# Kernel tuning notes

Hardware: AMD Instinct MI355X
Metric: run time of the kernel (lower is better)

## Reference

```python
import jax, jax.numpy as jnp
import numpy as np

DIM = 512
HEADS = 8
HEAD_DIM = DIM // HEADS
SCALE = HEAD_DIM ** -0.5
GROUP1 = np.array([2, 3, 5, 6, 1, 4, 0, 7, 8, 9, 14, 15, 11, 12, 10, 13])
GROUP2 = np.array([0, 1, 2, 3, 5, 6, 4, 7])
EPS = 1e-5


def setup_inputs() -> dict:
    key = jax.random.key(0)
    ks = jax.random.split(key, 6)
    B, N, C = 4096, 16, DIM
    x = jax.random.normal(ks[0], (B, N, C), dtype=jnp.float32)
    w_q = jax.random.normal(ks[1], (C, C), dtype=jnp.float32) * 0.02
    w_kv = jax.random.normal(ks[2], (2 * C, C), dtype=jnp.float32) * 0.02
    w_proj = jax.random.normal(ks[3], (C, C), dtype=jnp.float32) * 0.02
    b_proj = jax.random.normal(ks[4], (C,), dtype=jnp.float32) * 0.02
    gamma = jnp.ones((C,), dtype=jnp.float32)
    beta = jnp.zeros((C,), dtype=jnp.float32)
    return {"x": x, "w_q": w_q, "w_kv": w_kv, "w_proj": w_proj,
            "b_proj": b_proj, "gamma": gamma, "beta": beta}


def _layernorm(x, gamma, beta):
    mu = jnp.mean(x, axis=-1, keepdims=True)
    var = jnp.mean(jnp.square(x - mu), axis=-1, keepdims=True)
    return (x - mu) * jax.lax.rsqrt(var + EPS) * gamma + beta


def _avg_pool_pairs(x):
    # x: (B, L, C) -> (B, L//2, C), AvgPool1d(kernel=2, stride=2) over L
    return 0.5 * (x[:, 0::2] + x[:, 1::2])


def reference(x, w_q, w_kv, w_proj, b_proj, gamma, beta):
    B, N, C = x.shape
    q = (x @ w_q.T).reshape(B, N, HEADS, HEAD_DIM).transpose(0, 2, 1, 3)  # (B,H,N,d)
    # gather + avgpool preprocessing
    p1 = _avg_pool_pairs(x[:, GROUP1])  # (B, 8, C)
    p2 = _avg_pool_pairs(x[:, GROUP2])  # (B, 4, C)
    pools = jnp.concatenate([x, p1, p2], axis=1)  # (B, N+12, C)
    pools = _layernorm(pools, gamma, beta)
    M = pools.shape[1]
    kv = (pools @ w_kv.T).reshape(B, M, 2, HEADS, HEAD_DIM).transpose(2, 0, 3, 1, 4)
    k, v = kv[0], kv[1]  # (B,H,M,d)
    attn = jax.nn.softmax(jnp.einsum('bhnd,bhmd->bhnm', q, k) * SCALE, axis=-1)
    out = jnp.einsum('bhnm,bhmd->bhnd', attn, v)  # (B,H,N,d)
    out = out.transpose(0, 2, 1, 3).reshape(B, N, C)
    return out @ w_proj.T + b_proj
```

## Files before the change

kernel.cpp:

```cpp
#include <hip/hip_runtime.h>
#include <hip/hip_bf16.h>
#include <cstdint>
#include <cstddef>


using bf16 = __hip_bfloat16;

#define B_SZ   4096
#define NTOK   16
#define CDIM   512
#define MPOOL  28
#define NHEAD  8
#define HDIM   64
#define LN_EPS 1e-5f
#define ATT_SCALE 0.125f

typedef short bf16x8 __attribute__((ext_vector_type(8)));
typedef float f32x4  __attribute__((ext_vector_type(4)));

__constant__ int c_g1[16] = {2,3,5,6,1,4,0,7,8,9,14,15,11,12,10,13};
__constant__ int c_g2[8]  = {0,1,2,3,5,6,4,7};

__device__ __forceinline__ unsigned short f2b(float f) {
    unsigned u = __float_as_uint(f);
    return (unsigned short)((u + 0x7FFFu + ((u >> 16) & 1u)) >> 16);
}

__device__ __forceinline__ void lds_cp16(const void* g, void* l) {
    __builtin_amdgcn_global_load_lds(
        (const __attribute__((address_space(1))) void*)g,
        (__attribute__((address_space(3))) void*)l, 16, 0, 0);
}

__global__ __launch_bounds__(256) void f32_to_bf16_kernel(
    const float* __restrict__ src, bf16* __restrict__ dst, int n8)
{
    const int i = blockIdx.x * 256 + threadIdx.x;
    if (i >= n8) return;
    const float4* p = (const float4*)(src + (size_t)i * 8);
    float4 a = p[0], b = p[1];
    uint4 pk;
    pk.x = (unsigned)f2b(a.x) | ((unsigned)f2b(a.y) << 16);
    pk.y = (unsigned)f2b(a.z) | ((unsigned)f2b(a.w) << 16);
    pk.z = (unsigned)f2b(b.x) | ((unsigned)f2b(b.y) << 16);
    pk.w = (unsigned)f2b(b.z) | ((unsigned)f2b(b.w) << 16);
    *(uint4*)(dst + (size_t)i * 8) = pk;
}

__global__ __launch_bounds__(256) void pools_ln_kernel(
    const float* __restrict__ x, const float* __restrict__ gamma,
    const float* __restrict__ beta, bf16* __restrict__ pools,
    bf16* __restrict__ xb)
{
    const int wave = threadIdx.x >> 6;
    const int lane = threadIdx.x & 63;
    const int row  = blockIdx.x * 4 + wave;
    const int b = row / MPOOL;
    const int m = row % MPOOL;
    const float* xb_src = x + (size_t)b * NTOK * CDIM;
    const int c0 = lane * 8;

    float v[8];
    if (m < 16) {
        const float4* p = (const float4*)(xb_src + m * CDIM + c0);
        float4 a = p[0], c = p[1];
        v[0]=a.x; v[1]=a.y; v[2]=a.z; v[3]=a.w;
        v[4]=c.x; v[5]=c.y; v[6]=c.z; v[7]=c.w;
        uint4 pk;
        pk.x = (unsigned)f2b(v[0]) | ((unsigned)f2b(v[1]) << 16);
        pk.y = (unsigned)f2b(v[2]) | ((unsigned)f2b(v[3]) << 16);
        pk.z = (unsigned)f2b(v[4]) | ((unsigned)f2b(v[5]) << 16);
        pk.w = (unsigned)f2b(v[6]) | ((unsigned)f2b(v[7]) << 16);
        *(uint4*)(xb + (size_t)b * NTOK * CDIM + (size_t)m * CDIM + c0) = pk;
    } else {
        int r0, r1;
        if (m < 24) { int j = m - 16; r0 = c_g1[2*j]; r1 = c_g1[2*j+1]; }
        else        { int j = m - 24; r0 = c_g2[2*j]; r1 = c_g2[2*j+1]; }
        const float4* p0 = (const float4*)(xb_src + r0 * CDIM + c0);
        const float4* p1 = (const float4*)(xb_src + r1 * CDIM + c0);
        float4 a0 = p0[0], a1 = p0[1];
        float4 b0 = p1[0], b1 = p1[1];
        v[0]=0.5f*(a0.x+b0.x); v[1]=0.5f*(a0.y+b0.y);
        v[2]=0.5f*(a0.z+b0.z); v[3]=0.5f*(a0.w+b0.w);
        v[4]=0.5f*(a1.x+b1.x); v[5]=0.5f*(a1.y+b1.y);
        v[6]=0.5f*(a1.z+b1.z); v[7]=0.5f*(a1.w+b1.w);
    }

    float s = 0.f, sq = 0.f;
#pragma unroll
    for (int j = 0; j < 8; ++j) { s += v[j]; sq += v[j]*v[j]; }
#pragma unroll
    for (int off = 1; off < 64; off <<= 1) {
        s  += __shfl_xor(s,  off, 64);
        sq += __shfl_xor(sq, off, 64);
    }
    const float mu   = s * (1.f / CDIM);
    const float var  = sq * (1.f / CDIM) - mu * mu;
    const float rstd = rsqrtf(var + LN_EPS);

    unsigned short o[8];
#pragma unroll
    for (int j = 0; j < 8; ++j) {
        float g  = gamma[c0 + j];
        float bb = beta[c0 + j];
        o[j] = f2b((v[j] - mu) * rstd * g + bb);
    }
    uint4 pk;
    pk.x = (unsigned)o[0] | ((unsigned)o[1] << 16);
    pk.y = (unsigned)o[2] | ((unsigned)o[3] << 16);
    pk.z = (unsigned)o[4] | ((unsigned)o[5] << 16);
    pk.w = (unsigned)o[6] | ((unsigned)o[7] << 16);
    *(uint4*)(pools + (size_t)row * CDIM + c0) = pk;
}

template<bool OUT_BF16, bool BIAS, int NBLK>
__global__ __launch_bounds__(512, 2) void gemm256_kernel(
    const bf16* __restrict__ A, const bf16* __restrict__ W,
    const float* __restrict__ bias, void* __restrict__ Cptr, int Ncols)
{
    constexpr int K  = 512;
    constexpr int NT = K / 32;
    extern __shared__ __align__(16) char ring[];

    const int tid = threadIdx.x;
    const int wv = tid >> 6, ln = tid & 63;
    const int wr = wv >> 2, wc = wv & 3;
    const int fr = ln & 15, kb = ln >> 4;

    const int p  = blockIdx.x;
    const int o  = p >> 3;
    const int mb = (o / NBLK) * 8 + (p & 7);
    const int nb = o % NBLK;
    const size_t m0 = (size_t)mb * 256;
    const size_t n0 = (size_t)nb * 256;

    const int srow = wv * 16 + (ln >> 2);
    const int scol = (((ln & 3) * 16) ^ (((ln >> 3) & 3) << 4)) >> 1;
    const bf16* Asrc0 = A + (m0 + srow) * K + scol;
    const bf16* Asrc1 = A + (m0 + 128 + srow) * K + scol;
    const bf16* Wsrc0 = W + (n0 + srow) * K + scol;
    const bf16* Wsrc1 = W + (n0 + 128 + srow) * K + scol;
    char* const ringc = ring;

    const int aswz  = ((fr >> 1) & 3) << 4;
    const int a_off = (wr * 128 + fr) * 64 + ((kb * 16) ^ aswz);
    const int b_off = 16384 + (wc * 64 + fr) * 64 + ((kb * 16) ^ aswz);

    f32x4 acc[8][4];
#pragma unroll
    for (int i = 0; i < 8; ++i)
#pragma unroll
    for (int j = 0; j < 4; ++j)
        acc[i][j] = f32x4{0.f, 0.f, 0.f, 0.f};

    auto STAGE = [&](int t) {
        char* base = ringc + (t & 3) * 32768 + wv * 1024;
        const int ko = t * 32;
        lds_cp16(Asrc0 + ko, base);
        lds_cp16(Asrc1 + ko, base + 8192);
        lds_cp16(Wsrc0 + ko, base + 16384);
        lds_cp16(Wsrc1 + ko, base + 16384 + 8192);
    };

    STAGE(0);
    STAGE(1);
    asm volatile("s_waitcnt vmcnt(4)" ::: "memory");
    __builtin_amdgcn_s_barrier();

#pragma unroll 1
    for (int t = 0; t < NT; ++t) {
        if (t + 2 < NT) STAGE(t + 2);
        const char* sa = ringc + (t & 3) * 32768;

        bf16x8 af[8], bfr[4];
#pragma unroll
        for (int mi = 0; mi < 8; ++mi)
            af[mi] = *(const bf16x8*)(sa + a_off + mi * 1024);
#pragma unroll
        for (int nj = 0; nj < 4; ++nj)
            bfr[nj] = *(const bf16x8*)(sa + b_off + nj * 1024);

#pragma unroll
        for (int mi = 0; mi < 8; ++mi)
#pragma unroll
        for (int nj = 0; nj < 4; ++nj)
            acc[mi][nj] = __builtin_amdgcn_mfma_f32_16x16x32_bf16(
                af[mi], bfr[nj], acc[mi][nj], 0, 0, 0);

        if (t + 2 < NT) { asm volatile("s_waitcnt vmcnt(4)" ::: "memory"); }
        else            { asm volatile("s_waitcnt vmcnt(0)" ::: "memory"); }
        __builtin_amdgcn_s_barrier();
    }

    const int orow0 = wr * 128 + kb * 4;
    const int ocol0 = wc * 64 + fr;
    float bv[4];
#pragma unroll
    for (int nj = 0; nj < 4; ++nj)
        bv[nj] = BIAS ? bias[n0 + ocol0 + nj * 16] : 0.f;
#pragma unroll
    for (int mi = 0; mi < 8; ++mi) {
        const size_t rbase = m0 + orow0 + mi * 16;
#pragma unroll
        for (int r = 0; r < 4; ++r) {
            const size_t rowoff = (rbase + r) * (size_t)Ncols + n0 + ocol0;
#pragma unroll
            for (int nj = 0; nj < 4; ++nj) {
                float v = acc[mi][nj][r] + bv[nj];
                if (OUT_BF16)
                    ((unsigned short*)Cptr)[rowoff + nj * 16] = f2b(v);
                else
                    ((float*)Cptr)[rowoff + nj * 16] = v;
            }
        }
    }
}

__global__ __launch_bounds__(256) void attn_kernel(
    const bf16* __restrict__ q, const bf16* __restrict__ kv,
    bf16* __restrict__ att)
{
    __shared__ unsigned short P_t[4][512];

    const int tid = threadIdx.x;
    const int wv = tid >> 6, ln = tid & 63;
    const int fr = ln & 15, kb = ln >> 4;
    const int wg = blockIdx.x * 4 + wv;
    const int b = wg >> 3, h = wg & 7;

    const bf16* qb = q  + (size_t)b * (NTOK * CDIM) + h * HDIM;
    const bf16* kp = kv + (size_t)b * (MPOOL * 2 * CDIM) + h * HDIM;
    const bf16* vp = kp + CDIM;

    bf16x8 aq[2];
#pragma unroll
    for (int ks = 0; ks < 2; ++ks)
        aq[ks] = *(const bf16x8*)(qb + fr * CDIM + ks * 32 + kb * 8);

    bf16x8 bk[2][2];
#pragma unroll
    for (int mt = 0; mt < 2; ++mt)
#pragma unroll
        for (int ks = 0; ks < 2; ++ks)
            bk[mt][ks] = *(const bf16x8*)(kp + (size_t)(mt * 16 + fr) * (2 * CDIM)
                                             + ks * 32 + kb * 8);

    const bf16* vlane = vp + (size_t)kb * 8 * (2 * CDIM) + fr;
    bf16x8 bv[4];
#pragma unroll
    for (int dt = 0; dt < 4; ++dt)
#pragma unroll
        for (int j = 0; j < 8; ++j)
            bv[dt][j] = *(const short*)(vlane + (size_t)j * (2 * CDIM) + dt * 16);

    f32x4 st0 = {0.f, 0.f, 0.f, 0.f}, st1 = {0.f, 0.f, 0.f, 0.f};
    st0 = __builtin_amdgcn_mfma_f32_16x16x32_bf16(aq[0], bk[0][0], st0, 0, 0, 0);
    st0 = __builtin_amdgcn_mfma_f32_16x16x32_bf16(aq[1], bk[0][1], st0, 0, 0, 0);
    st1 = __builtin_amdgcn_mfma_f32_16x16x32_bf16(aq[0], bk[1][0], st1, 0, 0, 0);
    st1 = __builtin_amdgcn_mfma_f32_16x16x32_bf16(aq[1], bk[1][1], st1, 0, 0, 0);

    const bool kmask = (fr >= MPOOL - 16);
#pragma unroll
    for (int r = 0; r < 4; ++r) {
        st0[r] *= ATT_SCALE;
        st1[r] = kmask ? -1e30f : st1[r] * ATT_SCALE;
    }

    float p0[4], p1[4];
#pragma unroll
    for (int r = 0; r < 4; ++r) {
        float mx = fmaxf(st0[r], st1[r]);
        mx = fmaxf(mx, __shfl_xor(mx, 1, 64));
        mx = fmaxf(mx, __shfl_xor(mx, 2, 64));
        mx = fmaxf(mx, __shfl_xor(mx, 4, 64));
        mx = fmaxf(mx, __shfl_xor(mx, 8, 64));
        float e0 = expf(st0[r] - mx);
        float e1 = expf(st1[r] - mx);
        float s = e0 + e1;
        s += __shfl_xor(s, 1, 64);
        s += __shfl_xor(s, 2, 64);
        s += __shfl_xor(s, 4, 64);
        s += __shfl_xor(s, 8, 64);
        const float inv = 1.f / s;
        p0[r] = e0 * inv;
        p1[r] = e1 * inv;
    }

    {
        ushort4 w0, w1;
        w0.x = f2b(p0[0]); w0.y = f2b(p0[1]); w0.z = f2b(p0[2]); w0.w = f2b(p0[3]);
        w1.x = f2b(p1[0]); w1.y = f2b(p1[1]); w1.z = f2b(p1[2]); w1.w = f2b(p1[3]);
        *(ushort4*)&P_t[wv][(fr)      * 16 + kb * 4] = w0;
        *(ushort4*)&P_t[wv][(16 + fr) * 16 + kb * 4] = w1;
    }
    asm volatile("s_waitcnt lgkmcnt(0)" ::: "memory");

    bf16x8 pa;
#pragma unroll
    for (int j = 0; j < 8; ++j)
        pa[j] = (short)P_t[wv][(kb * 8 + j) * 16 + fr];

    f32x4 o[4];
#pragma unroll
    for (int dt = 0; dt < 4; ++dt) {
        o[dt] = f32x4{0.f, 0.f, 0.f, 0.f};
        o[dt] = __builtin_amdgcn_mfma_f32_16x16x32_bf16(pa, bv[dt], o[dt], 0, 0, 0);
    }

    unsigned short* ob = (unsigned short*)(att + (size_t)b * (NTOK * CDIM) + h * HDIM);
#pragma unroll
    for (int r = 0; r < 4; ++r) {
        const size_t nrow = (size_t)(kb * 4 + r) * CDIM;
#pragma unroll
        for (int dt = 0; dt < 4; ++dt)
            ob[nrow + dt * 16 + fr] = f2b(o[dt][r]);
    }
}

extern "C" void kernel_launch(void* const* d_in, const int* in_sizes, int n_in,
                              void* d_out, int out_size, void* d_ws, size_t ws_size,
                              hipStream_t stream)
{
    const float* x      = (const float*)d_in[0];
    const float* w_q    = (const float*)d_in[1];
    const float* w_kv   = (const float*)d_in[2];
    const float* w_proj = (const float*)d_in[3];
    const float* b_proj = (const float*)d_in[4];
    const float* gamma  = (const float*)d_in[5];
    const float* beta   = (const float*)d_in[6];

    char* ws = (char*)d_ws;
    bf16* xb    = (bf16*)(ws);
    bf16* pools = (bf16*)(ws + 67108864ull);
    bf16* qbuf  = (bf16*)(ws + 67108864ull + 117440512ull);
    bf16* kvbuf = (bf16*)(ws + 67108864ull + 117440512ull + 67108864ull);
    bf16* wqb   = (bf16*)(ws + 67108864ull + 117440512ull + 67108864ull + 234881024ull);
    bf16* wkvb  = (bf16*)((char*)wqb + 524288ull);
    bf16* wpb   = (bf16*)((char*)wkvb + 1048576ull);
    bf16* atbuf = pools;

    hipFuncSetAttribute((const void*)gemm256_kernel<true, false, 2>,
                        hipFuncAttributeMaxDynamicSharedMemorySize, 131072);
    hipFuncSetAttribute((const void*)gemm256_kernel<true, false, 4>,
                        hipFuncAttributeMaxDynamicSharedMemorySize, 131072);
    hipFuncSetAttribute((const void*)gemm256_kernel<false, true, 2>,
                        hipFuncAttributeMaxDynamicSharedMemorySize, 131072);

    f32_to_bf16_kernel<<<128, 256, 0, stream>>>(w_q, wqb, 32768);
    f32_to_bf16_kernel<<<256, 256, 0, stream>>>(w_kv, wkvb, 65536);
    f32_to_bf16_kernel<<<128, 256, 0, stream>>>(w_proj, wpb, 32768);

    pools_ln_kernel<<<(B_SZ * MPOOL) / 4, 256, 0, stream>>>(x, gamma, beta, pools, xb);

    gemm256_kernel<true, false, 2><<<512, 512, 131072, stream>>>(
        xb, wqb, nullptr, (void*)qbuf, 512);

    gemm256_kernel<true, false, 4><<<1792, 512, 131072, stream>>>(
        pools, wkvb, nullptr, (void*)kvbuf, 1024);

    attn_kernel<<<(B_SZ * NHEAD) / 4, 256, 0, stream>>>(qbuf, kvbuf, atbuf);

    gemm256_kernel<false, true, 2><<<512, 512, 131072, stream>>>(
        atbuf, wpb, b_proj, d_out, 512);
}
```

Before: 432.3 us.

## Deepen GEMM LDS prefetch to three stages and split MFMA loop into halves

The GEMM main loop now prefetches three k-tiles ahead instead of two. Each iteration is split into two halves whose LDS fragment reads and global-to-LDS copies are interleaved with MFMA clusters. It adds s_setprio around the MFMA blocks and extra barriers to overlap memory traffic with matrix math. The cost is more barriers per iteration and tighter ring-buffer reuse across the 4-slot ring. It also adds an unused bf16-to-float helper.

```diff
diff --git a/kernel.cpp b/kernel.cpp
--- a/kernel.cpp
+++ b/kernel.cpp
@@ -21,6 +21,9 @@
 __constant__ int c_g1[16] = {2,3,5,6,1,4,0,7,8,9,14,15,11,12,10,13};
 __constant__ int c_g2[8]  = {0,1,2,3,5,6,4,7};
 
+__device__ __forceinline__ float us2f(unsigned short u) {
+    return __uint_as_float(((unsigned)u) << 16);
+}
 __device__ __forceinline__ unsigned short f2b(float f) {
     unsigned u = __float_as_uint(f);
     return (unsigned short)((u + 0x7FFFu + ((u >> 16) & 1u)) >> 16);
@@ -164,31 +167,66 @@
 
     STAGE(0);
     STAGE(1);
-    asm volatile("s_waitcnt vmcnt(4)" ::: "memory");
+    STAGE(2);
+    asm volatile("s_waitcnt vmcnt(8)" ::: "memory");
     __builtin_amdgcn_s_barrier();
 
 #pragma unroll 1
-    for (int t = 0; t < NT; ++t) {
-        if (t + 2 < NT) STAGE(t + 2);
-        const char* sa = ringc + (t & 3) * 32768;
-
-        bf16x8 af[8], bfr[4];
-#pragma unroll
-        for (int mi = 0; mi < 8; ++mi)
-            af[mi] = *(const bf16x8*)(sa + a_off + mi * 1024);
+    for (int u = 0; u < NT; ++u) {
+        const char* sa = ringc + (u & 3) * 32768;
+
+        bf16x8 afA[4], bfr[4];
+#pragma unroll
+        for (int mi = 0; mi < 4; ++mi)
+            afA[mi] = *(const bf16x8*)(sa + a_off + mi * 1024);
 #pragma unroll
         for (int nj = 0; nj < 4; ++nj)
             bfr[nj] = *(const bf16x8*)(sa + b_off + nj * 1024);
 
-#pragma unroll
-        for (int mi = 0; mi < 8; ++mi)
+        if (u + 3 < NT) {
+            char* base = ringc + ((u + 3) & 3) * 32768 + wv * 1024;
+            const int ko = (u + 3) * 32;
+            lds_cp16(Asrc0 + ko, base);
+            lds_cp16(Asrc1 + ko, base + 8192);
+        }
+
+        __builtin_amdgcn_s_barrier();
+        asm volatile("s_waitcnt lgkmcnt(0)" ::: "memory");
+        __builtin_amdgcn_s_setprio(1);
+#pragma unroll
+        for (int mi = 0; mi < 4; ++mi)
 #pragma unroll
         for (int nj = 0; nj < 4; ++nj)
             acc[mi][nj] = __builtin_amdgcn_mfma_f32_16x16x32_bf16(
-                af[mi], bfr[nj], acc[mi][nj], 0, 0, 0);
-
-        if (t + 2 < NT) { asm volatile("s_waitcnt vmcnt(4)" ::: "memory"); }
-        else            { asm volatile("s_waitcnt vmcnt(0)" ::: "memory"); }
+                afA[mi], bfr[nj], acc[mi][nj], 0, 0, 0);
+        __builtin_amdgcn_s_setprio(0);
+        __builtin_amdgcn_s_barrier();
+
+        bf16x8 afB[4];
+#pragma unroll
+        for (int mi = 0; mi < 4; ++mi)
+            afB[mi] = *(const bf16x8*)(sa + a_off + (4 + mi) * 1024);
+
+        if (u + 3 < NT) {
+            char* base = ringc + ((u + 3) & 3) * 32768 + wv * 1024;
+            const int ko = (u + 3) * 32;
+            lds_cp16(Wsrc0 + ko, base + 16384);
+            lds_cp16(Wsrc1 + ko, base + 16384 + 8192);
+        }
+
+        if (u <= NT - 4)      { asm volatile("s_waitcnt vmcnt(8)" ::: "memory"); }
+        else if (u == NT - 3) { asm volatile("s_waitcnt vmcnt(4)" ::: "memory"); }
+        else if (u == NT - 2) { asm volatile("s_waitcnt vmcnt(0)" ::: "memory"); }
+        __builtin_amdgcn_s_barrier();
+        asm volatile("s_waitcnt lgkmcnt(0)" ::: "memory");
+        __builtin_amdgcn_s_setprio(1);
+#pragma unroll
+        for (int mi = 0; mi < 4; ++mi)
+#pragma unroll
+        for (int nj = 0; nj < 4; ++nj)
+            acc[4 + mi][nj] = __builtin_amdgcn_mfma_f32_16x16x32_bf16(
+                afB[mi], bfr[nj], acc[4 + mi][nj], 0, 0, 0);
+        __builtin_amdgcn_s_setprio(0);
         __builtin_amdgcn_s_barrier();
     }
 
```

New measurement: 436.2 us. No clear change (+0.9%).

## Stage per-batch KV into swizzled LDS and map one block per batch

Applied to the files above, without the earlier changes.

The attention kernel now uses one 512-thread block per batch element, with one wave per head. The block copies that batch's 28x1024 KV rows into LDS with 16-byte async copies under an XOR swizzle, and zeroes the padding rows up to 32. K and V fragments are then read from LDS instead of strided global loads, and the per-element V gathers no longer hit global memory. This costs 72KB of dynamic LDS per block, which limits occupancy to two blocks per CU, and adds a block-wide barrier before compute.

```diff
diff --git a/kernel.cpp b/kernel.cpp
--- a/kernel.cpp
+++ b/kernel.cpp
@@ -216,22 +216,33 @@
     }
 }
 
-__global__ __launch_bounds__(256) void attn_kernel(
+__global__ __launch_bounds__(512, 2) void attn_kernel(
     const bf16* __restrict__ q, const bf16* __restrict__ kv,
     bf16* __restrict__ att)
 {
-    __shared__ unsigned short P_t[4][512];
+    extern __shared__ __align__(16) char smem[];
+    char* const kvl = smem;
+    unsigned short (*P_t)[512] = (unsigned short (*)[512])(smem + 65536);
 
     const int tid = threadIdx.x;
     const int wv = tid >> 6, ln = tid & 63;
     const int fr = ln & 15, kb = ln >> 4;
-    const int wg = blockIdx.x * 4 + wv;
-    const int b = wg >> 3, h = wg & 7;
-
-    const bf16* qb = q  + (size_t)b * (NTOK * CDIM) + h * HDIM;
-    const bf16* kp = kv + (size_t)b * (MPOOL * 2 * CDIM) + h * HDIM;
-    const bf16* vp = kp + CDIM;
-
+    const int b = blockIdx.x;
+    const int h = wv;
+
+    const char* kvg = (const char*)kv + (size_t)b * (MPOOL * 2 * CDIM * 2);
+#pragma unroll
+    for (int i = 0; i < 7; ++i) {
+        const int ob  = i * 8192 + wv * 1024;
+        const int row = ob >> 11;
+        const int x   = ((row & 7) << 4) ^ (((row >> 3) & 3) << 5);
+        const int src = ((ob & 2047) + ln * 16) ^ x;
+        lds_cp16(kvg + (size_t)row * 2048 + src, kvl + ob);
+    }
+    *(uint4*)(kvl + 57344 + tid * 16) = uint4{0u, 0u, 0u, 0u};
+    __syncthreads();
+
+    const bf16* qb = q + (size_t)b * (NTOK * CDIM) + h * HDIM;
     bf16x8 aq[2];
 #pragma unroll
     for (int ks = 0; ks < 2; ++ks)
@@ -239,19 +250,25 @@
 
     bf16x8 bk[2][2];
 #pragma unroll
-    for (int mt = 0; mt < 2; ++mt)
+    for (int mt = 0; mt < 2; ++mt) {
+        const int row = mt * 16 + fr;
+        const int x   = ((row & 7) << 4) ^ (((row >> 3) & 3) << 5);
 #pragma unroll
         for (int ks = 0; ks < 2; ++ks)
-            bk[mt][ks] = *(const bf16x8*)(kp + (size_t)(mt * 16 + fr) * (2 * CDIM)
-                                             + ks * 32 + kb * 8);
-
-    const bf16* vlane = vp + (size_t)kb * 8 * (2 * CDIM) + fr;
+            bk[mt][ks] = *(const bf16x8*)(kvl + row * 2048 +
+                              ((h * 128 + ks * 64 + kb * 16) ^ x));
+    }
+
     bf16x8 bv[4];
 #pragma unroll
     for (int dt = 0; dt < 4; ++dt)
 #pragma unroll
-        for (int j = 0; j < 8; ++j)
-            bv[dt][j] = *(const short*)(vlane + (size_t)j * (2 * CDIM) + dt * 16);
+        for (int j = 0; j < 8; ++j) {
+            const int row = kb * 8 + j;
+            const int x   = ((row & 7) << 4) ^ (((row >> 3) & 3) << 5);
+            bv[dt][j] = *(const short*)(kvl + row * 2048 +
+                              ((1024 + h * 128 + dt * 32 + fr * 2) ^ x));
+        }
 
     f32x4 st0 = {0.f, 0.f, 0.f, 0.f}, st1 = {0.f, 0.f, 0.f, 0.f};
     st0 = __builtin_amdgcn_mfma_f32_16x16x32_bf16(aq[0], bk[0][0], st0, 0, 0, 0);
@@ -345,6 +362,8 @@
                         hipFuncAttributeMaxDynamicSharedMemorySize, 131072);
     hipFuncSetAttribute((const void*)gemm256_kernel<false, true, 2>,
                         hipFuncAttributeMaxDynamicSharedMemorySize, 131072);
+    hipFuncSetAttribute((const void*)attn_kernel,
+                        hipFuncAttributeMaxDynamicSharedMemorySize, 73728);
 
     f32_to_bf16_kernel<<<128, 256, 0, stream>>>(w_q, wqb, 32768);
     f32_to_bf16_kernel<<<256, 256, 0, stream>>>(w_kv, wkvb, 65536);
@@ -358,7 +377,7 @@
     gemm256_kernel<true, false, 4><<<1792, 512, 131072, stream>>>(
         pools, wkvb, nullptr, (void*)kvbuf, 1024);
 
-    attn_kernel<<<(B_SZ * NHEAD) / 4, 256, 0, stream>>>(qbuf, kvbuf, atbuf);
+    attn_kernel<<<B_SZ, 512, 73728, stream>>>(qbuf, kvbuf, atbuf);
 
     gemm256_kernel<false, true, 2><<<512, 512, 131072, stream>>>(
         atbuf, wpb, b_proj, d_out, 512);
```

Result: faster. 422.6 us (-2.3%).
